# Optimization experiments

Measured on AMD Instinct MI355X. Metric: run time of the kernel, lower is better.

Reference implementation:

```python
import jax, jax.numpy as jnp
import numpy as np

D_MODEL = 1024
NUM_HEADS = 16
HEAD_DIM = D_MODEL // NUM_HEADS
BATCH = 2
SEQ = 2048


def setup_inputs() -> dict:
    key = jax.random.key(0)
    ks = jax.random.split(key, 9)
    s_in = 1.0 / np.sqrt(D_MODEL)  # kaiming-ish fan-in scaling for stability
    return {
        "x": jax.random.normal(ks[0], (BATCH, SEQ, D_MODEL), jnp.float32),
        "wq": jax.random.normal(ks[1], (D_MODEL, D_MODEL), jnp.float32) * s_in,
        "bq": jnp.zeros((D_MODEL,), jnp.float32),
        "wk": jax.random.normal(ks[2], (D_MODEL, D_MODEL), jnp.float32) * s_in,
        "bk": jnp.zeros((D_MODEL,), jnp.float32),
        "wv": jax.random.normal(ks[3], (D_MODEL, D_MODEL), jnp.float32) * s_in,
        "bv": jnp.zeros((D_MODEL,), jnp.float32),
        "wo": jax.random.normal(ks[4], (D_MODEL, D_MODEL), jnp.float32) * s_in,
        "bo": jnp.zeros((D_MODEL,), jnp.float32),
    }


def reference(x, wq, bq, wk, bk, wv, bv, wo, bo):
    B, S, _ = x.shape
    # QKV projections, split heads: [B, H, S, Dh]
    def proj(w, b):
        y = x @ w + b
        return y.reshape(B, S, NUM_HEADS, HEAD_DIM).transpose(0, 2, 1, 3)

    q = proj(wq, bq)
    k = proj(wk, bk)
    v = proj(wv, bv)

    scale = 1.0 / jnp.sqrt(jnp.float32(HEAD_DIM))
    scores = jnp.einsum("bhsd,bhtd->bhst", q, k) * scale  # [B,H,S,S]
    attn = jax.nn.softmax(scores, axis=-1)
    out = jnp.einsum("bhst,bhtd->bhsd", attn, v)  # [B,H,S,Dh]
    out = out.transpose(0, 2, 1, 3).reshape(B, S, D_MODEL)
    return out @ wo + bo
```

## Files before the change

kernel.cpp:

```cpp
#include <hip/hip_runtime.h>
#include <stdint.h>
#include <stddef.h>


typedef __attribute__((ext_vector_type(8))) short short8;
typedef __attribute__((ext_vector_type(4))) float f32x4;
typedef __attribute__((ext_vector_type(16))) float f32x16;
typedef __attribute__((ext_vector_type(4))) unsigned short u16x4;

#define MFMA16(a, b, c) __builtin_amdgcn_mfma_f32_16x16x32_bf16((a), (b), (c), 0, 0, 0)
#define MFMA32(a, b, c) __builtin_amdgcn_mfma_f32_32x32x16_bf16((a), (b), (c), 0, 0, 0)

__device__ __forceinline__ unsigned short f2bf(float f) {
  union { float f; unsigned u; } v; v.f = f;
  unsigned r = v.u + 0x7fffu + ((v.u >> 16) & 1u);
  return (unsigned short)(r >> 16);
}

__device__ __forceinline__ unsigned cvt_pk_bf16(float lo, float hi) {
  unsigned r;
  asm("v_cvt_pk_bf16_f32 %0, %1, %2" : "=v"(r) : "v"(lo), "v"(hi));
  return r;
}

__device__ __forceinline__ void pl32_swap(unsigned& a, unsigned& b) {
  asm volatile("v_permlane32_swap_b32 %0, %1" : "+v"(a), "+v"(b));
}

__device__ __forceinline__ short8 mk8(unsigned a, unsigned b, unsigned c, unsigned d) {
  union { unsigned u[4]; short8 s; } v;
  v.u[0] = a; v.u[1] = b; v.u[2] = c; v.u[3] = d;
  return v.s;
}

__global__ __launch_bounds__(256) void cast_x_kernel(const float* __restrict__ x,
                                                     unsigned short* __restrict__ xb) {
  int i = (blockIdx.x * 256 + threadIdx.x) * 4;
  float4 v = *reinterpret_cast<const float4*>(x + i);
  u16x4 o;
  o.x = f2bf(v.x); o.y = f2bf(v.y); o.z = f2bf(v.z); o.w = f2bf(v.w);
  *reinterpret_cast<u16x4*>(xb + i) = o;
}

__global__ __launch_bounds__(256) void prep_w_kernel(const float* __restrict__ wq,
                                                     const float* __restrict__ wk,
                                                     const float* __restrict__ wv,
                                                     const float* __restrict__ wo,
                                                     unsigned short* __restrict__ wt) {
  __shared__ unsigned short t_lds[32][33];
  int bid = blockIdx.x;
  int wsel = bid >> 10;
  int rem = bid & 1023;
  int kb = (rem >> 5) << 5;
  int nb = (rem & 31) << 5;
  const float* W = (wsel == 0) ? wq : (wsel == 1) ? wk : (wsel == 2) ? wv : wo;
  int t = threadIdx.x;
  int r = t >> 3, c = (t & 7) * 4;
  float4 v = *reinterpret_cast<const float4*>(W + (size_t)(kb + r) * 1024 + nb + c);
  t_lds[r][c + 0] = f2bf(v.x);
  t_lds[r][c + 1] = f2bf(v.y);
  t_lds[r][c + 2] = f2bf(v.z);
  t_lds[r][c + 3] = f2bf(v.w);
  __syncthreads();
  u16x4 o;
  o.x = t_lds[c + 0][r]; o.y = t_lds[c + 1][r];
  o.z = t_lds[c + 2][r]; o.w = t_lds[c + 3][r];
  *reinterpret_cast<u16x4*>(wt + (size_t)(wsel * 1024 + nb + r) * 1024 + kb + c) = o;
}

__global__ __launch_bounds__(256) void pack_bias_kernel(const float* __restrict__ bq,
                                                        const float* __restrict__ bk,
                                                        const float* __restrict__ bv,
                                                        float* __restrict__ bias3) {
  int i = blockIdx.x * 256 + threadIdx.x;
  if (i < 3072) bias3[i] = (i < 1024) ? bq[i] : (i < 2048) ? bk[i - 1024] : bv[i - 2048];
}

template <typename OutT, bool QS>
__global__ __launch_bounds__(256) void gemm_bt_kernel(const unsigned short* __restrict__ A,
                                                      const unsigned short* __restrict__ Bt,
                                                      const float* __restrict__ bias,
                                                      OutT* __restrict__ C, int N) {
  constexpr int K = 1024;
  __shared__ __align__(16) unsigned short a_lds[128 * 32];
  __shared__ __align__(16) unsigned short b_lds[128 * 32];
  const int nb = N >> 7;
  const int nwg = nb << 5;
  const int cpx = nwg >> 3;
  const int wg = ((int)blockIdx.x & 7) * cpx + ((int)blockIdx.x >> 3);
  const int bm = wg / nb;
  const int bn = wg % nb;
  const int m0 = bm << 7, n0 = bn << 7;
  const int tid = threadIdx.x;
  const int w = tid >> 6, l = tid & 63;
  const int lr = l & 15, lg = l >> 4;
  const int wm = (w >> 1) << 6, wn = (w & 1) << 6;

  const int q0 = w * 2, q1 = w * 2 + 1;
  const unsigned short* pa0 = A + (size_t)(m0 + q0 * 16 + (l >> 2)) * K + (l & 3) * 8;
  const unsigned short* pa1 = A + (size_t)(m0 + q1 * 16 + (l >> 2)) * K + (l & 3) * 8;
  const unsigned short* pb0 = Bt + (size_t)(n0 + q0 * 16 + (l >> 2)) * K + (l & 3) * 8;
  const unsigned short* pb1 = Bt + (size_t)(n0 + q1 * 16 + (l >> 2)) * K + (l & 3) * 8;

  f32x4 acc[4][4] = {};

  for (int k0 = 0; k0 < K; k0 += 32) {
    __syncthreads();
    __builtin_amdgcn_global_load_lds(
        (const __attribute__((address_space(1))) void*)(pa0 + k0),
        (__attribute__((address_space(3))) void*)(a_lds + q0 * 512), 16, 0, 0);
    __builtin_amdgcn_global_load_lds(
        (const __attribute__((address_space(1))) void*)(pa1 + k0),
        (__attribute__((address_space(3))) void*)(a_lds + q1 * 512), 16, 0, 0);
    __builtin_amdgcn_global_load_lds(
        (const __attribute__((address_space(1))) void*)(pb0 + k0),
        (__attribute__((address_space(3))) void*)(b_lds + q0 * 512), 16, 0, 0);
    __builtin_amdgcn_global_load_lds(
        (const __attribute__((address_space(1))) void*)(pb1 + k0),
        (__attribute__((address_space(3))) void*)(b_lds + q1 * 512), 16, 0, 0);
    __syncthreads();

    short8 af[4], bfr[4];
#pragma unroll
    for (int i = 0; i < 4; ++i)
      af[i] = *reinterpret_cast<const short8*>(a_lds + (wm + i * 16 + lr) * 32 + lg * 8);
#pragma unroll
    for (int i = 0; i < 4; ++i)
      bfr[i] = *reinterpret_cast<const short8*>(b_lds + (wn + i * 16 + lr) * 32 + lg * 8);
#pragma unroll
    for (int i = 0; i < 4; ++i)
#pragma unroll
      for (int j = 0; j < 4; ++j)
        acc[i][j] = MFMA16(af[i], bfr[j], acc[i][j]);
  }

  const float scale = (QS && n0 < 1024) ? 0.18033688011111f : 1.0f;
#pragma unroll
  for (int i = 0; i < 4; ++i) {
#pragma unroll
    for (int j = 0; j < 4; ++j) {
#pragma unroll
      for (int r = 0; r < 4; ++r) {
        int m = m0 + wm + i * 16 + lg * 4 + r;
        int n = n0 + wn + j * 16 + lr;
        float val = (acc[i][j][r] + bias[n]) * scale;
        if constexpr (sizeof(OutT) == 2) {
          C[(size_t)m * N + n] = (OutT)f2bf(val);
        } else {
          C[(size_t)m * N + n] = val;
        }
      }
    }
  }
}

__device__ __forceinline__ void stage_kv(char* kw, char* vw, int ktt, int kd0, int pi, int vd0,
                                         short8 k0, short8 k1, short8 va, short8 vb) {
  *reinterpret_cast<short8*>(kw + ktt * 128 + ((kd0 * 2) ^ ((ktt & 7) << 4))) = k0;
  *reinterpret_cast<short8*>(kw + (ktt + 32) * 128 + ((kd0 * 2) ^ ((ktt & 7) << 4))) = k1;
  union { short8 s; unsigned u[4]; } ua, ub;
  ua.s = va; ub.s = vb;
#pragma unroll
  for (int jr = 0; jr < 4; ++jr) {
    unsigned w0 = __builtin_amdgcn_perm(ub.u[jr], ua.u[jr], 0x05040100u);
    unsigned w1 = __builtin_amdgcn_perm(ub.u[jr], ua.u[jr], 0x07060302u);
    int d0 = vd0 + 2 * jr, d1 = d0 + 1;
    *reinterpret_cast<unsigned*>(vw + d0 * 128 + ((4 * pi) ^ ((d0 & 7) << 4))) = w0;
    *reinterpret_cast<unsigned*>(vw + d1 * 128 + ((4 * pi) ^ ((d1 & 7) << 4))) = w1;
  }
}

__global__ __launch_bounds__(256) void attn_kernel(const unsigned short* __restrict__ qkv,
                                                   unsigned short* __restrict__ aout) {
  __shared__ __align__(16) unsigned short k_lds[2][64 * 64];
  __shared__ __align__(16) unsigned short vt_lds[2][64 * 64];
  const int tid = threadIdx.x;
  const int w = tid >> 6, l = tid & 63;
  const int lq = l & 31;
  const int hi = l >> 5;
  const int wg = ((int)blockIdx.x & 7) * 64 + ((int)blockIdx.x >> 3);
  const int qblk = wg & 15;
  const int bh = wg >> 4;
  const int b = bh >> 4, h = bh & 15;
  const size_t rowbase = (size_t)b * 2048;
  const int q0 = qblk * 128 + w * 32;

  short8 qf[4];
  {
    const unsigned short* qrow = qkv + (rowbase + q0 + lq) * 3072 + h * 64 + hi * 8;
#pragma unroll
    for (int c = 0; c < 4; ++c)
      qf[c] = *reinterpret_cast<const short8*>(qrow + c * 16);
  }

  const unsigned short* kbase = qkv + rowbase * 3072 + 1024 + h * 64;
  const unsigned short* vbase = qkv + rowbase * 3072 + 2048 + h * 64;

  const int ktt = tid >> 3;
  const int kd0 = (tid & 7) * 8;
  const int pi = tid & 31;
  const int vd0 = (tid >> 5) * 8;
  const int swz_lq = (lq & 7) << 4;

  float ls0 = 0.f, ls1 = 0.f, ls2 = 0.f, ls3 = 0.f;
  f32x16 ot0 = {}, ot1 = {};

  short8 kpre0 = *reinterpret_cast<const short8*>(kbase + (size_t)ktt * 3072 + kd0);
  short8 kpre1 = *reinterpret_cast<const short8*>(kbase + (size_t)(ktt + 32) * 3072 + kd0);
  short8 vpa = *reinterpret_cast<const short8*>(vbase + (size_t)(2 * pi) * 3072 + vd0);
  short8 vpb = *reinterpret_cast<const short8*>(vbase + (size_t)(2 * pi + 1) * 3072 + vd0);
  stage_kv((char*)k_lds[0], (char*)vt_lds[0], ktt, kd0, pi, vd0, kpre0, kpre1, vpa, vpb);

  int cur = 0;
  for (int t0 = 0; t0 < 2048; t0 += 64) {
    __syncthreads();
    const bool more = (t0 + 64) < 2048;
    if (more) {
      kpre0 = *reinterpret_cast<const short8*>(kbase + (size_t)(t0 + 64 + ktt) * 3072 + kd0);
      kpre1 = *reinterpret_cast<const short8*>(kbase + (size_t)(t0 + 96 + ktt) * 3072 + kd0);
      vpa = *reinterpret_cast<const short8*>(vbase + (size_t)(t0 + 64 + 2 * pi) * 3072 + vd0);
      vpb = *reinterpret_cast<const short8*>(vbase + (size_t)(t0 + 65 + 2 * pi) * 3072 + vd0);
    }
    const char* kl = (const char*)k_lds[cur];
    const char* vl = (const char*)vt_lds[cur];

    f32x16 s0 = {}, s1 = {};
    __builtin_amdgcn_s_setprio(1);
#pragma unroll
    for (int c = 0; c < 4; ++c) {
      short8 kf0 = *reinterpret_cast<const short8*>(kl + lq * 128 + ((c * 32 + hi * 16) ^ swz_lq));
      short8 kf1 = *reinterpret_cast<const short8*>(kl + (32 + lq) * 128 + ((c * 32 + hi * 16) ^ swz_lq));
      s0 = MFMA32(kf0, qf[c], s0);
      s1 = MFMA32(kf1, qf[c], s1);
    }
    __builtin_amdgcn_s_setprio(0);

    if (more)
      stage_kv((char*)k_lds[cur ^ 1], (char*)vt_lds[cur ^ 1], ktt, kd0, pi, vd0,
               kpre0, kpre1, vpa, vpb);

    float p0[16], p1[16];
#pragma unroll
    for (int i = 0; i < 16; ++i) {
      p0[i] = __builtin_exp2f(s0[i]);
      if ((i & 3) == 0) ls0 += p0[i]; else if ((i & 3) == 1) ls1 += p0[i];
      else if ((i & 3) == 2) ls2 += p0[i]; else ls3 += p0[i];
    }
#pragma unroll
    for (int i = 0; i < 16; ++i) {
      p1[i] = __builtin_exp2f(s1[i]);
      if ((i & 3) == 0) ls0 += p1[i]; else if ((i & 3) == 1) ls1 += p1[i];
      else if ((i & 3) == 2) ls2 += p1[i]; else ls3 += p1[i];
    }

    short8 pf[4];
    {
      unsigned a0 = cvt_pk_bf16(p0[0], p0[1]),   a1 = cvt_pk_bf16(p0[4], p0[5]);
      unsigned b0 = cvt_pk_bf16(p0[2], p0[3]),   b1 = cvt_pk_bf16(p0[6], p0[7]);
      pl32_swap(a0, a1); pl32_swap(b0, b1);
      pf[0] = mk8(a0, b0, a1, b1);
      unsigned c0 = cvt_pk_bf16(p0[8], p0[9]),   c1 = cvt_pk_bf16(p0[12], p0[13]);
      unsigned d0 = cvt_pk_bf16(p0[10], p0[11]), d1 = cvt_pk_bf16(p0[14], p0[15]);
      pl32_swap(c0, c1); pl32_swap(d0, d1);
      pf[1] = mk8(c0, d0, c1, d1);
      unsigned e0 = cvt_pk_bf16(p1[0], p1[1]),   e1 = cvt_pk_bf16(p1[4], p1[5]);
      unsigned f0 = cvt_pk_bf16(p1[2], p1[3]),   f1 = cvt_pk_bf16(p1[6], p1[7]);
      pl32_swap(e0, e1); pl32_swap(f0, f1);
      pf[2] = mk8(e0, f0, e1, f1);
      unsigned g0 = cvt_pk_bf16(p1[8], p1[9]),   g1 = cvt_pk_bf16(p1[12], p1[13]);
      unsigned h0 = cvt_pk_bf16(p1[10], p1[11]), h1 = cvt_pk_bf16(p1[14], p1[15]);
      pl32_swap(g0, g1); pl32_swap(h0, h1);
      pf[3] = mk8(g0, h0, g1, h1);
    }

    __builtin_amdgcn_s_setprio(1);
#pragma unroll
    for (int c = 0; c < 4; ++c) {
      short8 vf0 = *reinterpret_cast<const short8*>(vl + lq * 128 + ((c * 32 + hi * 16) ^ swz_lq));
      short8 vf1 = *reinterpret_cast<const short8*>(vl + (32 + lq) * 128 + ((c * 32 + hi * 16) ^ swz_lq));
      ot0 = MFMA32(vf0, pf[c], ot0);
      ot1 = MFMA32(vf1, pf[c], ot1);
    }
    __builtin_amdgcn_s_setprio(0);
    cur ^= 1;
  }

  float lsum = (ls0 + ls1) + (ls2 + ls3);
  lsum += __shfl_xor(lsum, 32, 64);
  const float inv = 1.0f / lsum;
  __syncthreads();
  char* ob = (char*)k_lds + w * 4096;
#pragma unroll
  for (int r = 0; r < 16; r += 2) {
    int d = (r & 3) + 8 * (r >> 2) + 4 * hi;
    unsigned pk0 = cvt_pk_bf16(ot0[r] * inv, ot0[r + 1] * inv);
    *(unsigned*)(ob + lq * 128 + ((2 * d) ^ swz_lq)) = pk0;
    unsigned pk1 = cvt_pk_bf16(ot1[r] * inv, ot1[r + 1] * inv);
    *(unsigned*)(ob + lq * 128 + ((2 * (32 + d)) ^ swz_lq)) = pk1;
  }
  __syncthreads();
#pragma unroll
  for (int it = 0; it < 4; ++it) {
    int qq = it * 32 + (tid >> 3);
    int ch = tid & 7;
    const char* src = (const char*)k_lds + (qq >> 5) * 4096;
    short8 vv = *reinterpret_cast<const short8*>(
        src + (qq & 31) * 128 + ((ch * 16) ^ (((qq & 31) & 7) << 4)));
    *reinterpret_cast<short8*>(aout + (rowbase + qblk * 128 + qq) * 1024 + h * 64 + ch * 8) = vv;
  }
}

extern "C" void kernel_launch(void* const* d_in, const int* in_sizes, int n_in,
                              void* d_out, int out_size, void* d_ws, size_t ws_size,
                              hipStream_t stream) {
  const float* x  = (const float*)d_in[0];
  const float* wq = (const float*)d_in[1];
  const float* bq = (const float*)d_in[2];
  const float* wk = (const float*)d_in[3];
  const float* bk = (const float*)d_in[4];
  const float* wv = (const float*)d_in[5];
  const float* bv = (const float*)d_in[6];
  const float* wo = (const float*)d_in[7];
  const float* bo = (const float*)d_in[8];
  float* out = (float*)d_out;

  char* ws = (char*)d_ws;
  unsigned short* xb    = (unsigned short*)(ws);
  unsigned short* aob   = (unsigned short*)(ws);
  unsigned short* wt    = (unsigned short*)(ws + 8388608);
  float*          bias3 = (float*)(ws + 16777216);
  unsigned short* qkvb  = (unsigned short*)(ws + 16777216 + 16384);

  cast_x_kernel<<<4096, 256, 0, stream>>>(x, xb);
  prep_w_kernel<<<4096, 256, 0, stream>>>(wq, wk, wv, wo, wt);
  pack_bias_kernel<<<12, 256, 0, stream>>>(bq, bk, bv, bias3);

  gemm_bt_kernel<unsigned short, true><<<768, 256, 0, stream>>>(xb, wt, bias3, qkvb, 3072);

  attn_kernel<<<512, 256, 0, stream>>>(qkvb, aob);

  gemm_bt_kernel<float, false><<<256, 256, 0, stream>>>(aob, wt + (size_t)3072 * 1024, bo, out, 1024);
}
```

Baseline: 144.5 us.

## Double-buffer GEMM LDS tiles and stream K into attention LDS directly

The projection GEMM gets double-buffered LDS, so the next K-slice's global-to-LDS load is issued before the MFMAs on the current slice, leaving one barrier per iteration instead of two. The attention kernel loads K tiles with global_load_lds straight into LDS rather than through registers. It merges the K/V buffers into one LDS array with precomputed swizzled offsets and XOR buffer masks, and changes the swizzle pattern to (row&6). This removes register staging and VGPR pressure for K and one barrier per tile, at the cost of doubled GEMM LDS use and more complex addressing.

```diff
diff --git a/kernel.cpp b/kernel.cpp
--- a/kernel.cpp
+++ b/kernel.cpp
@@ -10,6 +10,8 @@
 
 #define MFMA16(a, b, c) __builtin_amdgcn_mfma_f32_16x16x32_bf16((a), (b), (c), 0, 0, 0)
 #define MFMA32(a, b, c) __builtin_amdgcn_mfma_f32_32x32x16_bf16((a), (b), (c), 0, 0, 0)
+#define AS1 __attribute__((address_space(1)))
+#define AS3 __attribute__((address_space(3)))
 
 __device__ __forceinline__ unsigned short f2bf(float f) {
   union { float f; unsigned u; } v; v.f = f;
@@ -82,8 +84,8 @@
                                                       const float* __restrict__ bias,
                                                       OutT* __restrict__ C, int N) {
   constexpr int K = 1024;
-  __shared__ __align__(16) unsigned short a_lds[128 * 32];
-  __shared__ __align__(16) unsigned short b_lds[128 * 32];
+  __shared__ __align__(16) unsigned short a_lds[2][128 * 32];
+  __shared__ __align__(16) unsigned short b_lds[2][128 * 32];
   const int nb = N >> 7;
   const int nwg = nb << 5;
   const int cpx = nwg >> 3;
@@ -102,37 +104,41 @@
   const unsigned short* pb0 = Bt + (size_t)(n0 + q0 * 16 + (l >> 2)) * K + (l & 3) * 8;
   const unsigned short* pb1 = Bt + (size_t)(n0 + q1 * 16 + (l >> 2)) * K + (l & 3) * 8;
 
+#define GEMM_STAGE(buf, k0)                                                        \
+  do {                                                                             \
+    __builtin_amdgcn_global_load_lds((const AS1 void*)(pa0 + (k0)),                \
+        (AS3 void*)(&a_lds[buf][q0 * 512]), 16, 0, 0);                             \
+    __builtin_amdgcn_global_load_lds((const AS1 void*)(pa1 + (k0)),                \
+        (AS3 void*)(&a_lds[buf][q1 * 512]), 16, 0, 0);                             \
+    __builtin_amdgcn_global_load_lds((const AS1 void*)(pb0 + (k0)),                \
+        (AS3 void*)(&b_lds[buf][q0 * 512]), 16, 0, 0);                             \
+    __builtin_amdgcn_global_load_lds((const AS1 void*)(pb1 + (k0)),                \
+        (AS3 void*)(&b_lds[buf][q1 * 512]), 16, 0, 0);                             \
+  } while (0)
+
   f32x4 acc[4][4] = {};
-
+  GEMM_STAGE(0, 0);
+  __syncthreads();
+
+  int cur = 0;
   for (int k0 = 0; k0 < K; k0 += 32) {
-    __syncthreads();
-    __builtin_amdgcn_global_load_lds(
-        (const __attribute__((address_space(1))) void*)(pa0 + k0),
-        (__attribute__((address_space(3))) void*)(a_lds + q0 * 512), 16, 0, 0);
-    __builtin_amdgcn_global_load_lds(
-        (const __attribute__((address_space(1))) void*)(pa1 + k0),
-        (__attribute__((address_space(3))) void*)(a_lds + q1 * 512), 16, 0, 0);
-    __builtin_amdgcn_global_load_lds(
-        (const __attribute__((address_space(1))) void*)(pb0 + k0),
-        (__attribute__((address_space(3))) void*)(b_lds + q0 * 512), 16, 0, 0);
-    __builtin_amdgcn_global_load_lds(
-        (const __attribute__((address_space(1))) void*)(pb1 + k0),
-        (__attribute__((address_space(3))) void*)(b_lds + q1 * 512), 16, 0, 0);
-    __syncthreads();
-
+    if (k0 + 32 < K) GEMM_STAGE(cur ^ 1, k0 + 32);
     short8 af[4], bfr[4];
 #pragma unroll
     for (int i = 0; i < 4; ++i)
-      af[i] = *reinterpret_cast<const short8*>(a_lds + (wm + i * 16 + lr) * 32 + lg * 8);
+      af[i] = *reinterpret_cast<const short8*>(&a_lds[cur][(wm + i * 16 + lr) * 32 + lg * 8]);
 #pragma unroll
     for (int i = 0; i < 4; ++i)
-      bfr[i] = *reinterpret_cast<const short8*>(b_lds + (wn + i * 16 + lr) * 32 + lg * 8);
+      bfr[i] = *reinterpret_cast<const short8*>(&b_lds[cur][(wn + i * 16 + lr) * 32 + lg * 8]);
 #pragma unroll
     for (int i = 0; i < 4; ++i)
 #pragma unroll
       for (int j = 0; j < 4; ++j)
         acc[i][j] = MFMA16(af[i], bfr[j], acc[i][j]);
-  }
+    __syncthreads();
+    cur ^= 1;
+  }
+#undef GEMM_STAGE
 
   const float scale = (QS && n0 < 1024) ? 0.18033688011111f : 1.0f;
 #pragma unroll
@@ -154,30 +160,12 @@
   }
 }
 
-__device__ __forceinline__ void stage_kv(char* kw, char* vw, int ktt, int kd0, int pi, int vd0,
-                                         short8 k0, short8 k1, short8 va, short8 vb) {
-  *reinterpret_cast<short8*>(kw + ktt * 128 + ((kd0 * 2) ^ ((ktt & 7) << 4))) = k0;
-  *reinterpret_cast<short8*>(kw + (ktt + 32) * 128 + ((kd0 * 2) ^ ((ktt & 7) << 4))) = k1;
-  union { short8 s; unsigned u[4]; } ua, ub;
-  ua.s = va; ub.s = vb;
-#pragma unroll
-  for (int jr = 0; jr < 4; ++jr) {
-    unsigned w0 = __builtin_amdgcn_perm(ub.u[jr], ua.u[jr], 0x05040100u);
-    unsigned w1 = __builtin_amdgcn_perm(ub.u[jr], ua.u[jr], 0x07060302u);
-    int d0 = vd0 + 2 * jr, d1 = d0 + 1;
-    *reinterpret_cast<unsigned*>(vw + d0 * 128 + ((4 * pi) ^ ((d0 & 7) << 4))) = w0;
-    *reinterpret_cast<unsigned*>(vw + d1 * 128 + ((4 * pi) ^ ((d1 & 7) << 4))) = w1;
-  }
-}
-
 __global__ __launch_bounds__(256) void attn_kernel(const unsigned short* __restrict__ qkv,
                                                    unsigned short* __restrict__ aout) {
-  __shared__ __align__(16) unsigned short k_lds[2][64 * 64];
-  __shared__ __align__(16) unsigned short vt_lds[2][64 * 64];
+  __shared__ __align__(16) char lds[32768];
   const int tid = threadIdx.x;
   const int w = tid >> 6, l = tid & 63;
-  const int lq = l & 31;
-  const int hi = l >> 5;
+  const int lq = l & 31, hi = l >> 5;
   const int wg = ((int)blockIdx.x & 7) * 64 + ((int)blockIdx.x >> 3);
   const int qblk = wg & 15;
   const int bh = wg >> 4;
@@ -193,51 +181,96 @@
       qf[c] = *reinterpret_cast<const short8*>(qrow + c * 16);
   }
 
-  const unsigned short* kbase = qkv + rowbase * 3072 + 1024 + h * 64;
-  const unsigned short* vbase = qkv + rowbase * 3072 + 2048 + h * 64;
-
-  const int ktt = tid >> 3;
-  const int kd0 = (tid & 7) * 8;
+  const int r0 = 16 * w + (l >> 3);
+  const int r1 = r0 + 8;
+  const char* kq0_src = (const char*)(qkv + rowbase * 3072 + 1024 + h * 64) +
+                        (size_t)r0 * 6144 + ((16 * (l & 7)) ^ ((r0 & 6) << 4));
+  const char* kq1_src = (const char*)(qkv + rowbase * 3072 + 1024 + h * 64) +
+                        (size_t)r1 * 6144 + ((16 * (l & 7)) ^ ((r1 & 6) << 4));
+  const int kdst0 = 2 * w * 1024;
+  const int kdst1 = kdst0 + 1024;
+
   const int pi = tid & 31;
   const int vd0 = (tid >> 5) * 8;
-  const int swz_lq = (lq & 7) << 4;
+  const unsigned short* vptr_a = qkv + (rowbase + 2 * pi) * 3072 + 2048 + h * 64 + vd0;
+  const unsigned short* vptr_b = vptr_a + 3072;
+
+  int aoff[4];
+#pragma unroll
+  for (int c = 0; c < 4; ++c)
+    aoff[c] = lq * 128 + ((c * 32 + hi * 16) ^ ((lq & 6) << 4));
+  int vwoff[4];
+#pragma unroll
+  for (int jr = 0; jr < 4; ++jr)
+    vwoff[jr] = 16384 + (vd0 + 2 * jr) * 128 + ((4 * pi) ^ ((2 * jr) << 4));
 
   float ls0 = 0.f, ls1 = 0.f, ls2 = 0.f, ls3 = 0.f;
   f32x16 ot0 = {}, ot1 = {};
 
-  short8 kpre0 = *reinterpret_cast<const short8*>(kbase + (size_t)ktt * 3072 + kd0);
-  short8 kpre1 = *reinterpret_cast<const short8*>(kbase + (size_t)(ktt + 32) * 3072 + kd0);
-  short8 vpa = *reinterpret_cast<const short8*>(vbase + (size_t)(2 * pi) * 3072 + vd0);
-  short8 vpb = *reinterpret_cast<const short8*>(vbase + (size_t)(2 * pi + 1) * 3072 + vd0);
-  stage_kv((char*)k_lds[0], (char*)vt_lds[0], ktt, kd0, pi, vd0, kpre0, kpre1, vpa, vpb);
+  __builtin_amdgcn_global_load_lds((const AS1 void*)kq0_src, (AS3 void*)(lds + kdst0), 16, 0, 0);
+  __builtin_amdgcn_global_load_lds((const AS1 void*)kq1_src, (AS3 void*)(lds + kdst1), 16, 0, 0);
+  kq0_src += 393216; kq1_src += 393216;
+  {
+    short8 va = *reinterpret_cast<const short8*>(vptr_a);
+    short8 vb = *reinterpret_cast<const short8*>(vptr_b);
+    vptr_a += 64 * 3072; vptr_b += 64 * 3072;
+    union { short8 s; unsigned u[4]; } ua, ub;
+    ua.s = va; ub.s = vb;
+#pragma unroll
+    for (int jr = 0; jr < 4; ++jr) {
+      unsigned w0 = __builtin_amdgcn_perm(ub.u[jr], ua.u[jr], 0x05040100u);
+      unsigned w1 = __builtin_amdgcn_perm(ub.u[jr], ua.u[jr], 0x07060302u);
+      *reinterpret_cast<unsigned*>(lds + vwoff[jr]) = w0;
+      *reinterpret_cast<unsigned*>(lds + vwoff[jr] + 128) = w1;
+    }
+  }
+  __syncthreads();
 
   int cur = 0;
   for (int t0 = 0; t0 < 2048; t0 += 64) {
-    __syncthreads();
     const bool more = (t0 + 64) < 2048;
+    const int bmask = cur << 13;
+    const int nmask = bmask ^ 8192;
+    short8 va, vb;
     if (more) {
-      kpre0 = *reinterpret_cast<const short8*>(kbase + (size_t)(t0 + 64 + ktt) * 3072 + kd0);
-      kpre1 = *reinterpret_cast<const short8*>(kbase + (size_t)(t0 + 96 + ktt) * 3072 + kd0);
-      vpa = *reinterpret_cast<const short8*>(vbase + (size_t)(t0 + 64 + 2 * pi) * 3072 + vd0);
-      vpb = *reinterpret_cast<const short8*>(vbase + (size_t)(t0 + 65 + 2 * pi) * 3072 + vd0);
-    }
-    const char* kl = (const char*)k_lds[cur];
-    const char* vl = (const char*)vt_lds[cur];
+      __builtin_amdgcn_global_load_lds((const AS1 void*)kq0_src,
+                                       (AS3 void*)(lds + nmask + kdst0), 16, 0, 0);
+      __builtin_amdgcn_global_load_lds((const AS1 void*)kq1_src,
+                                       (AS3 void*)(lds + nmask + kdst1), 16, 0, 0);
+      kq0_src += 393216; kq1_src += 393216;
+      va = *reinterpret_cast<const short8*>(vptr_a);
+      vb = *reinterpret_cast<const short8*>(vptr_b);
+      vptr_a += 64 * 3072; vptr_b += 64 * 3072;
+    }
+
+    const char* fb0 = lds + (aoff[0] ^ bmask);
+    const char* fb1 = lds + (aoff[1] ^ bmask);
+    const char* fb2 = lds + (aoff[2] ^ bmask);
+    const char* fb3 = lds + (aoff[3] ^ bmask);
 
     f32x16 s0 = {}, s1 = {};
     __builtin_amdgcn_s_setprio(1);
-#pragma unroll
-    for (int c = 0; c < 4; ++c) {
-      short8 kf0 = *reinterpret_cast<const short8*>(kl + lq * 128 + ((c * 32 + hi * 16) ^ swz_lq));
-      short8 kf1 = *reinterpret_cast<const short8*>(kl + (32 + lq) * 128 + ((c * 32 + hi * 16) ^ swz_lq));
-      s0 = MFMA32(kf0, qf[c], s0);
-      s1 = MFMA32(kf1, qf[c], s1);
-    }
+    s0 = MFMA32(*reinterpret_cast<const short8*>(fb0), qf[0], s0);
+    s1 = MFMA32(*reinterpret_cast<const short8*>(fb0 + 4096), qf[0], s1);
+    s0 = MFMA32(*reinterpret_cast<const short8*>(fb1), qf[1], s0);
+    s1 = MFMA32(*reinterpret_cast<const short8*>(fb1 + 4096), qf[1], s1);
+    s0 = MFMA32(*reinterpret_cast<const short8*>(fb2), qf[2], s0);
+    s1 = MFMA32(*reinterpret_cast<const short8*>(fb2 + 4096), qf[2], s1);
+    s0 = MFMA32(*reinterpret_cast<const short8*>(fb3), qf[3], s0);
+    s1 = MFMA32(*reinterpret_cast<const short8*>(fb3 + 4096), qf[3], s1);
     __builtin_amdgcn_s_setprio(0);
 
-    if (more)
-      stage_kv((char*)k_lds[cur ^ 1], (char*)vt_lds[cur ^ 1], ktt, kd0, pi, vd0,
-               kpre0, kpre1, vpa, vpb);
+    if (more) {
+      union { short8 s; unsigned u[4]; } ua, ub;
+      ua.s = va; ub.s = vb;
+#pragma unroll
+      for (int jr = 0; jr < 4; ++jr) {
+        unsigned w0 = __builtin_amdgcn_perm(ub.u[jr], ua.u[jr], 0x05040100u);
+        unsigned w1 = __builtin_amdgcn_perm(ub.u[jr], ua.u[jr], 0x07060302u);
+        *reinterpret_cast<unsigned*>(lds + (vwoff[jr] ^ nmask) - 16384 + 16384) = w0;
+        *reinterpret_cast<unsigned*>(lds + (vwoff[jr] ^ nmask) + 128) = w1;
+      }
+    }
 
     float p0[16], p1[16];
 #pragma unroll
@@ -274,22 +307,25 @@
     }
 
     __builtin_amdgcn_s_setprio(1);
-#pragma unroll
-    for (int c = 0; c < 4; ++c) {
-      short8 vf0 = *reinterpret_cast<const short8*>(vl + lq * 128 + ((c * 32 + hi * 16) ^ swz_lq));
-      short8 vf1 = *reinterpret_cast<const short8*>(vl + (32 + lq) * 128 + ((c * 32 + hi * 16) ^ swz_lq));
-      ot0 = MFMA32(vf0, pf[c], ot0);
-      ot1 = MFMA32(vf1, pf[c], ot1);
-    }
+    ot0 = MFMA32(*reinterpret_cast<const short8*>(fb0 + 16384), pf[0], ot0);
+    ot1 = MFMA32(*reinterpret_cast<const short8*>(fb0 + 20480), pf[0], ot1);
+    ot0 = MFMA32(*reinterpret_cast<const short8*>(fb1 + 16384), pf[1], ot0);
+    ot1 = MFMA32(*reinterpret_cast<const short8*>(fb1 + 20480), pf[1], ot1);
+    ot0 = MFMA32(*reinterpret_cast<const short8*>(fb2 + 16384), pf[2], ot0);
+    ot1 = MFMA32(*reinterpret_cast<const short8*>(fb2 + 20480), pf[2], ot1);
+    ot0 = MFMA32(*reinterpret_cast<const short8*>(fb3 + 16384), pf[3], ot0);
+    ot1 = MFMA32(*reinterpret_cast<const short8*>(fb3 + 20480), pf[3], ot1);
     __builtin_amdgcn_s_setprio(0);
+
+    __syncthreads();
     cur ^= 1;
   }
 
   float lsum = (ls0 + ls1) + (ls2 + ls3);
   lsum += __shfl_xor(lsum, 32, 64);
   const float inv = 1.0f / lsum;
-  __syncthreads();
-  char* ob = (char*)k_lds + w * 4096;
+  char* ob = lds + w * 4096;
+  const int swz_lq = (lq & 6) << 4;
 #pragma unroll
   for (int r = 0; r < 16; r += 2) {
     int d = (r & 3) + 8 * (r >> 2) + 4 * hi;
@@ -303,9 +339,9 @@
   for (int it = 0; it < 4; ++it) {
     int qq = it * 32 + (tid >> 3);
     int ch = tid & 7;
-    const char* src = (const char*)k_lds + (qq >> 5) * 4096;
+    const char* src = lds + (qq >> 5) * 4096;
     short8 vv = *reinterpret_cast<const short8*>(
-        src + (qq & 31) * 128 + ((ch * 16) ^ (((qq & 31) & 7) << 4)));
+        src + (qq & 31) * 128 + ((ch * 16) ^ (((qq & 31) & 6) << 4)));
     *reinterpret_cast<short8*>(aout + (rowbase + qblk * 128 + qq) * 1024 + h * 64 + ch * 8) = vv;
   }
 }
```

Result: faster. 141.3 us (-2.2%).

## Split attention over KV halves with merge kernel, double-buffer GEMM LDS loads

Applied to the files above, without the earlier changes.

Attention now optionally splits the key/value sequence into two halves across twice as many workgroups. Each workgroup writes unnormalized fp16 partial outputs and row sums, and a new merge kernel adds the partials, normalizes and writes bf16. Row sums are now computed with an MFMA against a ones vector instead of scalar adds. The GEMM gets double-buffered LDS with prefetch of the next k-slice. The split works without a max-subtraction rescale, so it relies on no running max being kept. It adds fp16 intermediate traffic and an extra launch, and picks the split path from the workspace size.

```diff
diff --git a/kernel.cpp b/kernel.cpp
--- a/kernel.cpp
+++ b/kernel.cpp
@@ -7,9 +7,12 @@
 typedef __attribute__((ext_vector_type(4))) float f32x4;
 typedef __attribute__((ext_vector_type(16))) float f32x16;
 typedef __attribute__((ext_vector_type(4))) unsigned short u16x4;
+typedef _Float16 h4 __attribute__((ext_vector_type(4)));
 
 #define MFMA16(a, b, c) __builtin_amdgcn_mfma_f32_16x16x32_bf16((a), (b), (c), 0, 0, 0)
 #define MFMA32(a, b, c) __builtin_amdgcn_mfma_f32_32x32x16_bf16((a), (b), (c), 0, 0, 0)
+#define AS1 __attribute__((address_space(1)))
+#define AS3 __attribute__((address_space(3)))
 
 __device__ __forceinline__ unsigned short f2bf(float f) {
   union { float f; unsigned u; } v; v.f = f;
@@ -82,8 +85,8 @@
                                                       const float* __restrict__ bias,
                                                       OutT* __restrict__ C, int N) {
   constexpr int K = 1024;
-  __shared__ __align__(16) unsigned short a_lds[128 * 32];
-  __shared__ __align__(16) unsigned short b_lds[128 * 32];
+  __shared__ __align__(16) unsigned short a_lds[2][128 * 32];
+  __shared__ __align__(16) unsigned short b_lds[2][128 * 32];
   const int nb = N >> 7;
   const int nwg = nb << 5;
   const int cpx = nwg >> 3;
@@ -102,37 +105,41 @@
   const unsigned short* pb0 = Bt + (size_t)(n0 + q0 * 16 + (l >> 2)) * K + (l & 3) * 8;
   const unsigned short* pb1 = Bt + (size_t)(n0 + q1 * 16 + (l >> 2)) * K + (l & 3) * 8;
 
+#define GEMM_STAGE(buf, k0)                                                        \
+  do {                                                                             \
+    __builtin_amdgcn_global_load_lds((const AS1 void*)(pa0 + (k0)),                \
+        (AS3 void*)(&a_lds[buf][q0 * 512]), 16, 0, 0);                             \
+    __builtin_amdgcn_global_load_lds((const AS1 void*)(pa1 + (k0)),                \
+        (AS3 void*)(&a_lds[buf][q1 * 512]), 16, 0, 0);                             \
+    __builtin_amdgcn_global_load_lds((const AS1 void*)(pb0 + (k0)),                \
+        (AS3 void*)(&b_lds[buf][q0 * 512]), 16, 0, 0);                             \
+    __builtin_amdgcn_global_load_lds((const AS1 void*)(pb1 + (k0)),                \
+        (AS3 void*)(&b_lds[buf][q1 * 512]), 16, 0, 0);                             \
+  } while (0)
+
   f32x4 acc[4][4] = {};
-
+  GEMM_STAGE(0, 0);
+  __syncthreads();
+
+  int cur = 0;
   for (int k0 = 0; k0 < K; k0 += 32) {
-    __syncthreads();
-    __builtin_amdgcn_global_load_lds(
-        (const __attribute__((address_space(1))) void*)(pa0 + k0),
-        (__attribute__((address_space(3))) void*)(a_lds + q0 * 512), 16, 0, 0);
-    __builtin_amdgcn_global_load_lds(
-        (const __attribute__((address_space(1))) void*)(pa1 + k0),
-        (__attribute__((address_space(3))) void*)(a_lds + q1 * 512), 16, 0, 0);
-    __builtin_amdgcn_global_load_lds(
-        (const __attribute__((address_space(1))) void*)(pb0 + k0),
-        (__attribute__((address_space(3))) void*)(b_lds + q0 * 512), 16, 0, 0);
-    __builtin_amdgcn_global_load_lds(
-        (const __attribute__((address_space(1))) void*)(pb1 + k0),
-        (__attribute__((address_space(3))) void*)(b_lds + q1 * 512), 16, 0, 0);
-    __syncthreads();
-
+    if (k0 + 32 < K) GEMM_STAGE(cur ^ 1, k0 + 32);
     short8 af[4], bfr[4];
 #pragma unroll
     for (int i = 0; i < 4; ++i)
-      af[i] = *reinterpret_cast<const short8*>(a_lds + (wm + i * 16 + lr) * 32 + lg * 8);
+      af[i] = *reinterpret_cast<const short8*>(&a_lds[cur][(wm + i * 16 + lr) * 32 + lg * 8]);
 #pragma unroll
     for (int i = 0; i < 4; ++i)
-      bfr[i] = *reinterpret_cast<const short8*>(b_lds + (wn + i * 16 + lr) * 32 + lg * 8);
+      bfr[i] = *reinterpret_cast<const short8*>(&b_lds[cur][(wn + i * 16 + lr) * 32 + lg * 8]);
 #pragma unroll
     for (int i = 0; i < 4; ++i)
 #pragma unroll
       for (int j = 0; j < 4; ++j)
         acc[i][j] = MFMA16(af[i], bfr[j], acc[i][j]);
-  }
+    __syncthreads();
+    cur ^= 1;
+  }
+#undef GEMM_STAGE
 
   const float scale = (QS && n0 < 1024) ? 0.18033688011111f : 1.0f;
 #pragma unroll
@@ -170,17 +177,23 @@
   }
 }
 
-__global__ __launch_bounds__(256) void attn_kernel(const unsigned short* __restrict__ qkv,
-                                                   unsigned short* __restrict__ aout) {
+template <int S>
+__global__ __launch_bounds__(256, 4) void attn_kernel(const unsigned short* __restrict__ qkv,
+                                                      _Float16* __restrict__ poA,
+                                                      _Float16* __restrict__ poB,
+                                                      float* __restrict__ pl) {
+  constexpr int TLEN = 2048 / S;
   __shared__ __align__(16) unsigned short k_lds[2][64 * 64];
   __shared__ __align__(16) unsigned short vt_lds[2][64 * 64];
   const int tid = threadIdx.x;
   const int w = tid >> 6, l = tid & 63;
   const int lq = l & 31;
   const int hi = l >> 5;
-  const int wg = ((int)blockIdx.x & 7) * 64 + ((int)blockIdx.x >> 3);
-  const int qblk = wg & 15;
-  const int bh = wg >> 4;
+  const int nwg = 512 * S;
+  const int wg = ((int)blockIdx.x & 7) * (nwg >> 3) + ((int)blockIdx.x >> 3);
+  int bh, qblk, kv;
+  if (S == 2) { bh = wg >> 5; qblk = (wg >> 1) & 15; kv = wg & 1; }
+  else        { bh = wg >> 4; qblk = wg & 15;        kv = 0; }
   const int b = bh >> 4, h = bh & 15;
   const size_t rowbase = (size_t)b * 2048;
   const int q0 = qblk * 128 + w * 32;
@@ -193,8 +206,8 @@
       qf[c] = *reinterpret_cast<const short8*>(qrow + c * 16);
   }
 
-  const unsigned short* kbase = qkv + rowbase * 3072 + 1024 + h * 64;
-  const unsigned short* vbase = qkv + rowbase * 3072 + 2048 + h * 64;
+  const unsigned short* kbase = qkv + (rowbase + kv * TLEN) * 3072 + 1024 + h * 64;
+  const unsigned short* vbase = qkv + (rowbase + kv * TLEN) * 3072 + 2048 + h * 64;
 
   const int ktt = tid >> 3;
   const int kd0 = (tid & 7) * 8;
@@ -202,8 +215,14 @@
   const int vd0 = (tid >> 5) * 8;
   const int swz_lq = (lq & 7) << 4;
 
-  float ls0 = 0.f, ls1 = 0.f, ls2 = 0.f, ls3 = 0.f;
-  f32x16 ot0 = {}, ot1 = {};
+  short8 ones;
+  {
+    union { unsigned u[4]; short8 s; } o_;
+    o_.u[0] = o_.u[1] = o_.u[2] = o_.u[3] = 0x3F803F80u;
+    ones = o_.s;
+  }
+
+  f32x16 ot0 = {}, ot1 = {}, lacc = {};
 
   short8 kpre0 = *reinterpret_cast<const short8*>(kbase + (size_t)ktt * 3072 + kd0);
   short8 kpre1 = *reinterpret_cast<const short8*>(kbase + (size_t)(ktt + 32) * 3072 + kd0);
@@ -212,9 +231,9 @@
   stage_kv((char*)k_lds[0], (char*)vt_lds[0], ktt, kd0, pi, vd0, kpre0, kpre1, vpa, vpb);
 
   int cur = 0;
-  for (int t0 = 0; t0 < 2048; t0 += 64) {
+  for (int t0 = 0; t0 < TLEN; t0 += 64) {
     __syncthreads();
-    const bool more = (t0 + 64) < 2048;
+    const bool more = (t0 + 64) < TLEN;
     if (more) {
       kpre0 = *reinterpret_cast<const short8*>(kbase + (size_t)(t0 + 64 + ktt) * 3072 + kd0);
       kpre1 = *reinterpret_cast<const short8*>(kbase + (size_t)(t0 + 96 + ktt) * 3072 + kd0);
@@ -241,17 +260,9 @@
 
     float p0[16], p1[16];
 #pragma unroll
-    for (int i = 0; i < 16; ++i) {
-      p0[i] = __builtin_exp2f(s0[i]);
-      if ((i & 3) == 0) ls0 += p0[i]; else if ((i & 3) == 1) ls1 += p0[i];
-      else if ((i & 3) == 2) ls2 += p0[i]; else ls3 += p0[i];
-    }
-#pragma unroll
-    for (int i = 0; i < 16; ++i) {
-      p1[i] = __builtin_exp2f(s1[i]);
-      if ((i & 3) == 0) ls0 += p1[i]; else if ((i & 3) == 1) ls1 += p1[i];
-      else if ((i & 3) == 2) ls2 += p1[i]; else ls3 += p1[i];
-    }
+    for (int i = 0; i < 16; ++i) p0[i] = __builtin_exp2f(s0[i]);
+#pragma unroll
+    for (int i = 0; i < 16; ++i) p1[i] = __builtin_exp2f(s1[i]);
 
     short8 pf[4];
     {
@@ -280,34 +291,68 @@
       short8 vf1 = *reinterpret_cast<const short8*>(vl + (32 + lq) * 128 + ((c * 32 + hi * 16) ^ swz_lq));
       ot0 = MFMA32(vf0, pf[c], ot0);
       ot1 = MFMA32(vf1, pf[c], ot1);
+      lacc = MFMA32(ones, pf[c], lacc);
     }
     __builtin_amdgcn_s_setprio(0);
     cur ^= 1;
   }
 
-  float lsum = (ls0 + ls1) + (ls2 + ls3);
-  lsum += __shfl_xor(lsum, 32, 64);
-  const float inv = 1.0f / lsum;
+  const int g = bh * 16 + qblk;
+  _Float16* pop = (kv == 0 ? poA : poB) + (size_t)g * 8192;
+#pragma unroll
+  for (int r = 0; r < 16; ++r) {
+    int d = (r & 3) + 8 * (r >> 2) + 4 * hi;
+    pop[d * 128 + w * 32 + lq] = (_Float16)ot0[r];
+    pop[(32 + d) * 128 + w * 32 + lq] = (_Float16)ot1[r];
+  }
+  if (hi == 0) pl[(size_t)(g * S + kv) * 128 + w * 32 + lq] = lacc[0];
+}
+
+template <int S>
+__global__ __launch_bounds__(256) void merge_kernel(const _Float16* __restrict__ poA,
+                                                    const _Float16* __restrict__ poB,
+                                                    const float* __restrict__ pl,
+                                                    unsigned short* __restrict__ aout) {
+  __shared__ unsigned short lo[128][72];
+  const int g = blockIdx.x;
+  const int bh = g >> 4, qblk = g & 15;
+  const int b = bh >> 4, h = bh & 15;
+  const int tid = threadIdx.x;
+  const int qi = (tid & 31) * 4;
+  const int dg = tid >> 5;
+  const _Float16* P0 = poA + (size_t)g * 8192;
+  const _Float16* P1 = poB + (size_t)g * 8192;
+  const float* L = pl + (size_t)g * S * 128;
+
+  float inv[4];
+#pragma unroll
+  for (int j = 0; j < 4; ++j) {
+    float lv = L[qi + j];
+    if (S == 2) lv += L[128 + qi + j];
+    inv[j] = 1.0f / lv;
+  }
+#pragma unroll
+  for (int dd = 0; dd < 8; ++dd) {
+    int d = dg * 8 + dd;
+    h4 a = *reinterpret_cast<const h4*>(P0 + d * 128 + qi);
+    float o[4];
+#pragma unroll
+    for (int j = 0; j < 4; ++j) o[j] = (float)a[j];
+    if (S == 2) {
+      h4 bb = *reinterpret_cast<const h4*>(P1 + d * 128 + qi);
+#pragma unroll
+      for (int j = 0; j < 4; ++j) o[j] += (float)bb[j];
+    }
+#pragma unroll
+    for (int j = 0; j < 4; ++j) lo[qi + j][d] = f2bf(o[j] * inv[j]);
+  }
   __syncthreads();
-  char* ob = (char*)k_lds + w * 4096;
-#pragma unroll
-  for (int r = 0; r < 16; r += 2) {
-    int d = (r & 3) + 8 * (r >> 2) + 4 * hi;
-    unsigned pk0 = cvt_pk_bf16(ot0[r] * inv, ot0[r + 1] * inv);
-    *(unsigned*)(ob + lq * 128 + ((2 * d) ^ swz_lq)) = pk0;
-    unsigned pk1 = cvt_pk_bf16(ot1[r] * inv, ot1[r + 1] * inv);
-    *(unsigned*)(ob + lq * 128 + ((2 * (32 + d)) ^ swz_lq)) = pk1;
-  }
-  __syncthreads();
-#pragma unroll
-  for (int it = 0; it < 4; ++it) {
-    int qq = it * 32 + (tid >> 3);
-    int ch = tid & 7;
-    const char* src = (const char*)k_lds + (qq >> 5) * 4096;
-    short8 vv = *reinterpret_cast<const short8*>(
-        src + (qq & 31) * 128 + ((ch * 16) ^ (((qq & 31) & 7) << 4)));
-    *reinterpret_cast<short8*>(aout + (rowbase + qblk * 128 + qq) * 1024 + h * 64 + ch * 8) = vv;
-  }
+  const int q = tid >> 1, c0 = (tid & 1) * 32;
+  unsigned short* orow = aout + (size_t)(b * 2048 + qblk * 128 + q) * 1024 + h * 64 + c0;
+#pragma unroll
+  for (int k = 0; k < 4; ++k)
+    *reinterpret_cast<short8*>(orow + k * 8) =
+        *reinterpret_cast<const short8*>(&lo[q][c0 + k * 8]);
 }
 
 extern "C" void kernel_launch(void* const* d_in, const int* in_sizes, int n_in,
@@ -326,10 +371,14 @@
 
   char* ws = (char*)d_ws;
   unsigned short* xb    = (unsigned short*)(ws);
-  unsigned short* aob   = (unsigned short*)(ws);
+  _Float16*       poA   = (_Float16*)(ws);
   unsigned short* wt    = (unsigned short*)(ws + 8388608);
   float*          bias3 = (float*)(ws + 16777216);
-  unsigned short* qkvb  = (unsigned short*)(ws + 16777216 + 16384);
+  unsigned short* qkvb  = (unsigned short*)(ws + 16842752);
+  unsigned short* aob   = qkvb;
+  _Float16*       poB   = (_Float16*)(ws + 42008576);
+  const bool s2 = ws_size >= (size_t)51500000;
+  float* pl = (float*)(s2 ? (ws + 50397184) : (ws + 42008576));
 
   cast_x_kernel<<<4096, 256, 0, stream>>>(x, xb);
   prep_w_kernel<<<4096, 256, 0, stream>>>(wq, wk, wv, wo, wt);
@@ -337,7 +386,13 @@
 
   gemm_bt_kernel<unsigned short, true><<<768, 256, 0, stream>>>(xb, wt, bias3, qkvb, 3072);
 
-  attn_kernel<<<512, 256, 0, stream>>>(qkvb, aob);
+  if (s2) {
+    attn_kernel<2><<<1024, 256, 0, stream>>>(qkvb, poA, poB, pl);
+    merge_kernel<2><<<512, 256, 0, stream>>>(poA, poB, pl, aob);
+  } else {
+    attn_kernel<1><<<512, 256, 0, stream>>>(qkvb, poA, poB, pl);
+    merge_kernel<1><<<512, 256, 0, stream>>>(poA, poB, pl, aob);
+  }
 
   gemm_bt_kernel<float, false><<<256, 256, 0, stream>>>(aob, wt + (size_t)3072 * 1024, bo, out, 1024);
 }
```

New measurement: 164.6 us. 13.9% more time.
